# Kernel optimization log

Measured on AMD Instinct MI355X. Metric: run time of the kernel, lower is better.

## Reference

```python
import jax, jax.numpy as jnp
import numpy as np

D = 1024; NH = 16; HD = D // NH; B = 2; L = 2048
BASE_FAST = (1.0 + 5.0 ** 0.5) / 2.0
BASE_SLOW = 1618.0
BASE_GLU = 16180.0
ALPHA_ATTN = 0.42; ALPHA_MLP = 1.07; ALPHA_ADV = 1.0
H_GATE = max(8, D // 4)   # rope_gate hidden
H_NU = max(4, D // 8)     # DuplexViscosity hidden
LN_EPS = 1e-5


def _rope_cos_sin(seq_len, dim, base, dtype=jnp.float32):
    idx = jnp.arange(0, dim, 2, dtype=dtype) / float(dim)
    inv = 1.0 / (base ** idx)
    t = jnp.arange(seq_len, dtype=dtype)
    freqs = jnp.outer(t, inv)                       # (L, D/2)
    emb = jnp.concatenate([freqs, freqs], axis=-1)  # (L, D)
    return jnp.cos(emb)[None], jnp.sin(emb)[None]   # (1, L, D)


def _rotate_half(x):
    x1, x2 = jnp.split(x, 2, axis=-1)
    return jnp.concatenate([-x2, x1], axis=-1)


def _apply_rope(x, cos, sin):
    return x * cos + _rotate_half(x) * sin


def setup_inputs() -> dict:
    key = jax.random.key(0)
    ks = jax.random.split(key, 16)
    std = 0.02
    # all Linear weights stored as (in, out) so forward is x @ W + b
    return {
        "z": jax.random.normal(ks[0], (B, L, D), jnp.float32),
        "Wq": jax.random.normal(ks[1], (D, D), jnp.float32) * std,
        "bq": jnp.zeros((D,), jnp.float32),
        "Wk": jax.random.normal(ks[2], (D, D), jnp.float32) * std,
        "bk": jnp.zeros((D,), jnp.float32),
        "Wv": jax.random.normal(ks[3], (D, D), jnp.float32) * std,
        "bv": jnp.zeros((D,), jnp.float32),
        "Wcoh": jax.random.normal(ks[4], (D, D), jnp.float32) * std,
        "gamma": jnp.zeros((1,), jnp.float32),
        "rg_w1": jax.random.normal(ks[5], (D, H_GATE), jnp.float32) * std,
        "rg_b1": jnp.zeros((H_GATE,), jnp.float32),
        "rg_w2": jax.random.normal(ks[6], (H_GATE, 1), jnp.float32) * std,
        "rg_b2": jnp.zeros((1,), jnp.float32),
        "nu_diff": jnp.asarray(0.2, jnp.float32),
        "nu_adv": jnp.asarray(0.01, jnp.float32),
        "nu_w1": jax.random.normal(ks[7], (D, H_NU), jnp.float32) * std,
        "nu_b1": jnp.zeros((H_NU,), jnp.float32),
        "nu_w2": jax.random.normal(ks[8], (H_NU, 1), jnp.float32) * std,
        "nu_b2": jnp.zeros((1,), jnp.float32),
        "Wu": jax.random.normal(ks[9], (D, D), jnp.float32) * std,
        "bu": jnp.zeros((D,), jnp.float32),
        "Wg": jax.random.normal(ks[10], (D, D), jnp.float32) * std,
        "bg": jnp.zeros((D,), jnp.float32),
        "ln_w": jnp.ones((D,), jnp.float32),
        "ln_b": jnp.zeros((D,), jnp.float32),
        "Cw": jax.random.normal(ks[11], (D, D), jnp.float32) * std,
        "Cb": jnp.zeros((D,), jnp.float32),
    }


def reference(z, Wq, bq, Wk, bk, Wv, bv, Wcoh, gamma, rg_w1, rg_b1, rg_w2, rg_b2,
              nu_diff, nu_adv, nu_w1, nu_b1, nu_w2, nu_b2, Wu, bu, Wg, bg,
              ln_w, ln_b, Cw, Cb):
    b, l, d = z.shape
    dt = z.dtype
    # causal cumulative mean pool[t] = mean(z[0..t])
    pool = jnp.cumsum(z, axis=1) / jnp.arange(1, l + 1, dtype=dt)[None, :, None]

    # QKV projections
    Q = z @ Wq + bq
    K_raw = z @ Wk + bk
    V = z @ Wv + bv

    # global coherence bias: (B, Lq, Lk)
    gk = pool @ Wcoh
    gb = jnp.einsum('bld,bmd->blm', gk, K_raw) * (d ** -0.5)
    gb = jnp.tanh(gamma[0]) * gb

    # hybrid RoPE gate (small MLP on pool, exact gelu as in torch)
    gate = jax.nn.sigmoid(jax.nn.gelu(pool @ rg_w1 + rg_b1, approximate=False) @ rg_w2 + rg_b2)  # (B,L,1)
    cos_f, sin_f = _rope_cos_sin(l, d, BASE_FAST, dt)
    cos_s, sin_s = _rope_cos_sin(l, d, BASE_SLOW, dt)
    cos = gate * cos_f + (1.0 - gate) * cos_s
    sin = gate * sin_f + (1.0 - gate) * sin_s
    Qr = _apply_rope(Q, cos, sin)
    Kr = _apply_rope(K_raw, cos, sin)

    # multi-head causal attention with fused coherence bias
    Qh = Qr.reshape(b, l, NH, HD).transpose(0, 2, 1, 3)
    Kh = Kr.reshape(b, l, NH, HD).transpose(0, 2, 1, 3)
    Vh = V.reshape(b, l, NH, HD).transpose(0, 2, 1, 3)
    logits = jnp.einsum('bhld,bhmd->bhlm', Qh, Kh) * (HD ** -0.5)
    logits = logits + gb[:, None]
    causal = jnp.tril(jnp.ones((l, l), bool))
    logits = jnp.where(causal[None, None], logits, -jnp.inf)
    attn = jax.nn.softmax(logits, axis=-1)
    attn_out = jnp.einsum('bhlm,bhmd->bhld', attn, Vh).transpose(0, 2, 1, 3).reshape(b, l, d)
    attn_w = attn.mean(axis=1)

    # DuplexViscosity on causal pool
    delta = jnp.tanh(jnp.tanh(pool @ nu_w1 + nu_b1) @ nu_w2 + nu_b2) * jnp.abs(nu_adv)
    nu_b = jnp.abs(nu_diff) + delta  # (B,L,1)

    # GLU branch with fixed slow-base RoPE
    cos_g, sin_g = _rope_cos_sin(l, d, BASE_GLU, dt)
    z_glu = _apply_rope(z, cos_g, sin_g)
    bilinear = (z_glu @ Wu + bu) * (z_glu @ Wg + bg)
    adv = -(ALPHA_ADV * nu_b) * bilinear
    mu = adv.mean(axis=-1, keepdims=True)
    var = ((adv - mu) ** 2).mean(axis=-1, keepdims=True)
    adv_n = (adv - mu) * jax.lax.rsqrt(var + LN_EPS) * ln_w + ln_b
    mlp_out = adv_n @ Cw + Cb

    z_next = z + ALPHA_ATTN * attn_out + ALPHA_MLP * mlp_out
    return z_next, attn_w
```

## Files before the change

### kernel.cpp

```cpp
#include <hip/hip_runtime.h>

#define DD 1024
#define NHH 16
#define HDD 64
#define BB 2
#define LL 2048
#define MM (BB*LL)
#define HG 256
#define HN 128

#define LOG_FAST 0.48121182f
#define LOG_SLOW 7.3889461f
#define LOG_GLU  9.6915312f
#define SCL 0.18033688f

typedef __attribute__((ext_vector_type(8))) short short8;
typedef __attribute__((ext_vector_type(4))) float f32x4;

__device__ __forceinline__ float gelu_f(float x) {
    return 0.5f * x * (1.0f + erff(x * 0.70710678f));
}

__device__ __forceinline__ ushort f2b(float x) {
    unsigned u = __float_as_uint(x);
    unsigned r = (u + 0x7FFFu + ((u >> 16) & 1u)) >> 16;
    return (ushort)r;
}

__device__ __forceinline__ float b2f(ushort x) {
    return __uint_as_float(((unsigned)x) << 16);
}

__device__ __forceinline__ void gl_lds16(const ushort* g, ushort* l) {
    __builtin_amdgcn_global_load_lds(
        (const __attribute__((address_space(1))) unsigned int*)g,
        (__attribute__((address_space(3))) unsigned int*)l, 16, 0, 0);
}

#define SWZC(row, c8) (((((row) << 3) | ((c8) ^ ((row) & 7)))) << 3)

__device__ __forceinline__ void stage_tile(const ushort* gsrc, int rstride,
                                           ushort* lds, int tid) {
    int wid = tid >> 6;
#pragma unroll
    for (int r = 0; r < 2; ++r) {
        int c = r * 256 + tid;
        int row = c >> 3;
        int c8 = (c & 7) ^ (row & 7);
        gl_lds16(gsrc + (size_t)row * rstride + c8 * 8,
                 lds + (size_t)(r * 256 + wid * 64) * 8);
    }
}

#define LCH 128
#define NCH 16
__global__ void pool_scan1(const float* __restrict__ z, float* __restrict__ part,
                           float* __restrict__ ctot, ushort* __restrict__ zb) {
    int ch = blockIdx.x, dg = blockIdx.y, b = blockIdx.z;
    int d = dg * 256 + threadIdx.x;
    size_t base = ((size_t)b * LL + ch * LCH) * DD + d;
    const float* zp = z + base;
    float* pp = part + base;
    ushort* zo = zb + base;
    float s = 0.f;
    for (int t = 0; t < LCH; ++t) {
        float v = zp[(size_t)t * DD];
        s += v;
        pp[(size_t)t * DD] = s;
        zo[(size_t)t * DD] = f2b(v);
    }
    ctot[((size_t)b * NCH + ch) * DD + d] = s;
}
__global__ void pool_scan2(const float* __restrict__ part, const float* __restrict__ ctot,
                           ushort* __restrict__ poolb) {
    int ch = blockIdx.x, dg = blockIdx.y, b = blockIdx.z;
    int d = dg * 256 + threadIdx.x;
    float off = 0.f;
    for (int c = 0; c < ch; ++c) off += ctot[((size_t)b * NCH + c) * DD + d];
    int t0 = ch * LCH;
    size_t base = ((size_t)b * LL + t0) * DD + d;
    const float* pp = part + base;
    ushort* po = poolb + base;
    for (int t = 0; t < LCH; ++t) {
        po[(size_t)t * DD] = f2b((pp[(size_t)t * DD] + off) / (float)(t0 + t + 1));
    }
}

__global__ void f2bT4_kernel(const float* __restrict__ W0, const float* __restrict__ W1,
                             const float* __restrict__ W2, const float* __restrict__ W3,
                             ushort* __restrict__ Wt) {
    const float* W = blockIdx.z == 0 ? W0 : (blockIdx.z == 1 ? W1 :
                     (blockIdx.z == 2 ? W2 : W3));
    ushort* dst = Wt + (size_t)blockIdx.z * 1024 * 1024;
    __shared__ float t[32][33];
    int n0 = blockIdx.x * 32, k0 = blockIdx.y * 32;
    int tx = threadIdx.x & 31, ty = threadIdx.x >> 5;
#pragma unroll
    for (int j = 0; j < 4; ++j)
        t[ty + j * 8][tx] = W[(size_t)(k0 + ty + j * 8) * 1024 + n0 + tx];
    __syncthreads();
#pragma unroll
    for (int j = 0; j < 4; ++j)
        dst[(size_t)(n0 + ty + j * 8) * 1024 + k0 + tx] = f2b(t[tx][ty + j * 8]);
}

__global__ void f2bT_rgnu(const float* __restrict__ Wrg, const float* __restrict__ Wnu,
                          ushort* __restrict__ WtRG, ushort* __restrict__ WtNU) {
    int zc = blockIdx.z;
    if (zc == 1 && blockIdx.x >= 4) return;
    const float* W = zc == 0 ? Wrg : Wnu;
    ushort* dst = zc == 0 ? WtRG : WtNU;
    int Ndim = zc == 0 ? HG : HN;
    __shared__ float t[32][33];
    int n0 = blockIdx.x * 32, k0 = blockIdx.y * 32;
    int tx = threadIdx.x & 31, ty = threadIdx.x >> 5;
#pragma unroll
    for (int j = 0; j < 4; ++j)
        t[ty + j * 8][tx] = W[(size_t)(k0 + ty + j * 8) * Ndim + n0 + tx];
    __syncthreads();
#pragma unroll
    for (int j = 0; j < 4; ++j)
        dst[(size_t)(n0 + ty + j * 8) * 1024 + k0 + tx] = f2b(t[tx][ty + j * 8]);
}

__global__ void f2bT3_kernel(const float* __restrict__ W0, const float* __restrict__ W1,
                             const float* __restrict__ W2, ushort* __restrict__ Wt) {
    const float* W = blockIdx.z == 0 ? W0 : (blockIdx.z == 1 ? W1 : W2);
    ushort* dst = Wt + (size_t)blockIdx.z * 1024 * 1024;
    __shared__ float t[32][33];
    int n0 = blockIdx.x * 32, k0 = blockIdx.y * 32;
    int tx = threadIdx.x & 31, ty = threadIdx.x >> 5;
#pragma unroll
    for (int j = 0; j < 4; ++j)
        t[ty + j * 8][tx] = W[(size_t)(k0 + ty + j * 8) * 1024 + n0 + tx];
    __syncthreads();
#pragma unroll
    for (int j = 0; j < 4; ++j)
        dst[(size_t)(n0 + ty + j * 8) * 1024 + k0 + tx] = f2b(t[tx][ty + j * 8]);
}

__global__ __launch_bounds__(256) void gemm_mfma(
        const ushort* __restrict__ A, const ushort* __restrict__ Wt,
        const float* __restrict__ bias, float* __restrict__ C, int Ndim) {
    __shared__ ushort As[4096];
    __shared__ ushort Bs[4096];
    int tid = threadIdx.x;
    int wid = tid >> 6, lane = tid & 63;
    int n0 = blockIdx.x * 128, m0 = blockIdx.y * 128;
    int wm = wid >> 1, wn = wid & 1;
    int quad = lane >> 4, l16 = lane & 15;

    f32x4 acc[4][4];
#pragma unroll
    for (int mi = 0; mi < 4; ++mi)
#pragma unroll
        for (int ni = 0; ni < 4; ++ni) acc[mi][ni] = (f32x4){0.f, 0.f, 0.f, 0.f};

    int c0 = wid * 128 + lane;
    int c1 = c0 + 64;
    const ushort* Ag0 = A + (size_t)(m0 + (c0 & 127)) * 1024 + (c0 >> 7) * 8;
    const ushort* Ag1 = A + (size_t)(m0 + (c1 & 127)) * 1024 + (c1 >> 7) * 8;
    const ushort* Bg0 = Wt + (size_t)(n0 + (c0 & 127)) * 1024 + (c0 >> 7) * 8;
    const ushort* Bg1 = Wt + (size_t)(n0 + (c1 & 127)) * 1024 + (c1 >> 7) * 8;
    ushort* Al0 = As + wid * 1024;
    ushort* Al1 = As + wid * 1024 + 512;
    ushort* Bl0 = Bs + wid * 1024;
    ushort* Bl1 = Bs + wid * 1024 + 512;

    const ushort* a_rd = &As[(quad * 128 + wm * 64 + l16) * 8];
    const ushort* b_rd = &Bs[(quad * 128 + wn * 64 + l16) * 8];

    for (int kb = 0; kb < 1024; kb += 32) {
        gl_lds16(Ag0 + kb, Al0);
        gl_lds16(Ag1 + kb, Al1);
        gl_lds16(Bg0 + kb, Bl0);
        gl_lds16(Bg1 + kb, Bl1);
        __syncthreads();
        short8 af[4], bf[4];
#pragma unroll
        for (int mi = 0; mi < 4; ++mi)
            af[mi] = *(const short8*)(a_rd + mi * 16 * 8);
#pragma unroll
        for (int ni = 0; ni < 4; ++ni)
            bf[ni] = *(const short8*)(b_rd + ni * 16 * 8);
#pragma unroll
        for (int mi = 0; mi < 4; ++mi)
#pragma unroll
            for (int ni = 0; ni < 4; ++ni)
                acc[mi][ni] = __builtin_amdgcn_mfma_f32_16x16x32_bf16(
                    af[mi], bf[ni], acc[mi][ni], 0, 0, 0);
        __syncthreads();
    }
    int bcol[4];
    float bval[4];
#pragma unroll
    for (int ni = 0; ni < 4; ++ni) {
        bcol[ni] = n0 + wn * 64 + ni * 16 + l16;
        bval[ni] = bias ? bias[bcol[ni]] : 0.f;
    }
#pragma unroll
    for (int mi = 0; mi < 4; ++mi) {
#pragma unroll
        for (int r = 0; r < 4; ++r) {
            int row = m0 + wm * 64 + mi * 16 + quad * 4 + r;
            float* Cp = C + (size_t)row * Ndim;
#pragma unroll
            for (int ni = 0; ni < 4; ++ni)
                Cp[bcol[ni]] = acc[mi][ni][r] + bval[ni];
        }
    }
}

__global__ __launch_bounds__(256) void gemm_mfma3(
        const ushort* __restrict__ A, const ushort* __restrict__ Wt,
        const float* __restrict__ b0, const float* __restrict__ b1,
        const float* __restrict__ b2, float* __restrict__ C,
        ushort* __restrict__ K16r) {
    int zid = blockIdx.z;
    const ushort* W = Wt + (size_t)zid * 1024 * 1024;
    const float* bias = zid == 0 ? b0 : (zid == 1 ? b1 : b2);
    float* Cz = C + (size_t)zid * (size_t)MM * DD;
    __shared__ ushort As[4096];
    __shared__ ushort Bs[4096];
    int tid = threadIdx.x;
    int wid = tid >> 6, lane = tid & 63;
    int n0 = blockIdx.x * 128, m0 = blockIdx.y * 128;
    int wm = wid >> 1, wn = wid & 1;
    int quad = lane >> 4, l16 = lane & 15;

    f32x4 acc[4][4];
#pragma unroll
    for (int mi = 0; mi < 4; ++mi)
#pragma unroll
        for (int ni = 0; ni < 4; ++ni) acc[mi][ni] = (f32x4){0.f, 0.f, 0.f, 0.f};

    int c0 = wid * 128 + lane;
    int c1 = c0 + 64;
    const ushort* Ag0 = A + (size_t)(m0 + (c0 & 127)) * 1024 + (c0 >> 7) * 8;
    const ushort* Ag1 = A + (size_t)(m0 + (c1 & 127)) * 1024 + (c1 >> 7) * 8;
    const ushort* Bg0 = W + (size_t)(n0 + (c0 & 127)) * 1024 + (c0 >> 7) * 8;
    const ushort* Bg1 = W + (size_t)(n0 + (c1 & 127)) * 1024 + (c1 >> 7) * 8;
    ushort* Al0 = As + wid * 1024;
    ushort* Al1 = As + wid * 1024 + 512;
    ushort* Bl0 = Bs + wid * 1024;
    ushort* Bl1 = Bs + wid * 1024 + 512;

    const ushort* a_rd = &As[(quad * 128 + wm * 64 + l16) * 8];
    const ushort* b_rd = &Bs[(quad * 128 + wn * 64 + l16) * 8];

    for (int kb = 0; kb < 1024; kb += 32) {
        gl_lds16(Ag0 + kb, Al0);
        gl_lds16(Ag1 + kb, Al1);
        gl_lds16(Bg0 + kb, Bl0);
        gl_lds16(Bg1 + kb, Bl1);
        __syncthreads();
        short8 af[4], bf[4];
#pragma unroll
        for (int mi = 0; mi < 4; ++mi)
            af[mi] = *(const short8*)(a_rd + mi * 16 * 8);
#pragma unroll
        for (int ni = 0; ni < 4; ++ni)
            bf[ni] = *(const short8*)(b_rd + ni * 16 * 8);
#pragma unroll
        for (int mi = 0; mi < 4; ++mi)
#pragma unroll
            for (int ni = 0; ni < 4; ++ni)
                acc[mi][ni] = __builtin_amdgcn_mfma_f32_16x16x32_bf16(
                    af[mi], bf[ni], acc[mi][ni], 0, 0, 0);
        __syncthreads();
    }
    float bval[4];
    int bcol[4];
#pragma unroll
    for (int ni = 0; ni < 4; ++ni) {
        bcol[ni] = n0 + wn * 64 + ni * 16 + l16;
        bval[ni] = bias[bcol[ni]];
    }
    bool doK = (zid == 1) && (K16r != nullptr);
#pragma unroll
    for (int mi = 0; mi < 4; ++mi) {
#pragma unroll
        for (int r = 0; r < 4; ++r) {
            int row = m0 + wm * 64 + mi * 16 + quad * 4 + r;
            float* Cp = Cz + (size_t)row * 1024;
            ushort* Kp = K16r + (size_t)row * 1024;
#pragma unroll
            for (int ni = 0; ni < 4; ++ni) {
                float v = acc[mi][ni][r] + bval[ni];
                Cp[bcol[ni]] = v;
                if (doK) Kp[bcol[ni]] = f2b(v);
            }
        }
    }
}

__global__ __launch_bounds__(256) void gemm_mfma_b16out(
        const ushort* __restrict__ A, const ushort* __restrict__ Wt,
        ushort* __restrict__ C, int Ndim) {
    __shared__ ushort As[4096];
    __shared__ ushort Bs[4096];
    int tid = threadIdx.x;
    int wid = tid >> 6, lane = tid & 63;
    int n0 = blockIdx.x * 128, m0 = blockIdx.y * 128;
    int wm = wid >> 1, wn = wid & 1;
    int quad = lane >> 4, l16 = lane & 15;

    f32x4 acc[4][4];
#pragma unroll
    for (int mi = 0; mi < 4; ++mi)
#pragma unroll
        for (int ni = 0; ni < 4; ++ni) acc[mi][ni] = (f32x4){0.f, 0.f, 0.f, 0.f};

    int c0 = wid * 128 + lane;
    int c1 = c0 + 64;
    const ushort* Ag0 = A + (size_t)(m0 + (c0 & 127)) * 1024 + (c0 >> 7) * 8;
    const ushort* Ag1 = A + (size_t)(m0 + (c1 & 127)) * 1024 + (c1 >> 7) * 8;
    const ushort* Bg0 = Wt + (size_t)(n0 + (c0 & 127)) * 1024 + (c0 >> 7) * 8;
    const ushort* Bg1 = Wt + (size_t)(n0 + (c1 & 127)) * 1024 + (c1 >> 7) * 8;
    ushort* Al0 = As + wid * 1024;
    ushort* Al1 = As + wid * 1024 + 512;
    ushort* Bl0 = Bs + wid * 1024;
    ushort* Bl1 = Bs + wid * 1024 + 512;

    const ushort* a_rd = &As[(quad * 128 + wm * 64 + l16) * 8];
    const ushort* b_rd = &Bs[(quad * 128 + wn * 64 + l16) * 8];

    for (int kb = 0; kb < 1024; kb += 32) {
        gl_lds16(Ag0 + kb, Al0);
        gl_lds16(Ag1 + kb, Al1);
        gl_lds16(Bg0 + kb, Bl0);
        gl_lds16(Bg1 + kb, Bl1);
        __syncthreads();
        short8 af[4], bf[4];
#pragma unroll
        for (int mi = 0; mi < 4; ++mi)
            af[mi] = *(const short8*)(a_rd + mi * 16 * 8);
#pragma unroll
        for (int ni = 0; ni < 4; ++ni)
            bf[ni] = *(const short8*)(b_rd + ni * 16 * 8);
#pragma unroll
        for (int mi = 0; mi < 4; ++mi)
#pragma unroll
            for (int ni = 0; ni < 4; ++ni)
                acc[mi][ni] = __builtin_amdgcn_mfma_f32_16x16x32_bf16(
                    af[mi], bf[ni], acc[mi][ni], 0, 0, 0);
        __syncthreads();
    }
#pragma unroll
    for (int mi = 0; mi < 4; ++mi) {
#pragma unroll
        for (int r = 0; r < 4; ++r) {
            int row = m0 + wm * 64 + mi * 16 + quad * 4 + r;
            ushort* Cp = C + (size_t)row * Ndim;
#pragma unroll
            for (int ni = 0; ni < 4; ++ni)
                Cp[n0 + wn * 64 + ni * 16 + l16] = f2b(acc[mi][ni][r]);
        }
    }
}

__global__ __launch_bounds__(256) void gemm_gates(
        const ushort* __restrict__ A, const ushort* __restrict__ WtRG,
        const ushort* __restrict__ WtNU, const float* __restrict__ rg_b1,
        const float* __restrict__ nu_b1, float* __restrict__ H1,
        float* __restrict__ N1) {
    int bx = blockIdx.x;
    bool isH = bx < 2;
    const ushort* Wt = isH ? WtRG : WtNU;
    const float* bias = isH ? rg_b1 : nu_b1;
    float* C = isH ? H1 : N1;
    int Ndim = isH ? HG : HN;
    int n0 = isH ? bx * 128 : 0;
    int m0 = blockIdx.y * 128;
    __shared__ ushort As[4096];
    __shared__ ushort Bs[4096];
    int tid = threadIdx.x;
    int wid = tid >> 6, lane = tid & 63;
    int wm = wid >> 1, wn = wid & 1;
    int quad = lane >> 4, l16 = lane & 15;

    f32x4 acc[4][4];
#pragma unroll
    for (int mi = 0; mi < 4; ++mi)
#pragma unroll
        for (int ni = 0; ni < 4; ++ni) acc[mi][ni] = (f32x4){0.f, 0.f, 0.f, 0.f};

    int c0 = wid * 128 + lane;
    int c1 = c0 + 64;
    const ushort* Ag0 = A + (size_t)(m0 + (c0 & 127)) * 1024 + (c0 >> 7) * 8;
    const ushort* Ag1 = A + (size_t)(m0 + (c1 & 127)) * 1024 + (c1 >> 7) * 8;
    const ushort* Bg0 = Wt + (size_t)(n0 + (c0 & 127)) * 1024 + (c0 >> 7) * 8;
    const ushort* Bg1 = Wt + (size_t)(n0 + (c1 & 127)) * 1024 + (c1 >> 7) * 8;
    ushort* Al0 = As + wid * 1024;
    ushort* Al1 = As + wid * 1024 + 512;
    ushort* Bl0 = Bs + wid * 1024;
    ushort* Bl1 = Bs + wid * 1024 + 512;

    const ushort* a_rd = &As[(quad * 128 + wm * 64 + l16) * 8];
    const ushort* b_rd = &Bs[(quad * 128 + wn * 64 + l16) * 8];

    for (int kb = 0; kb < 1024; kb += 32) {
        gl_lds16(Ag0 + kb, Al0);
        gl_lds16(Ag1 + kb, Al1);
        gl_lds16(Bg0 + kb, Bl0);
        gl_lds16(Bg1 + kb, Bl1);
        __syncthreads();
        short8 af[4], bf[4];
#pragma unroll
        for (int mi = 0; mi < 4; ++mi)
            af[mi] = *(const short8*)(a_rd + mi * 16 * 8);
#pragma unroll
        for (int ni = 0; ni < 4; ++ni)
            bf[ni] = *(const short8*)(b_rd + ni * 16 * 8);
#pragma unroll
        for (int mi = 0; mi < 4; ++mi)
#pragma unroll
            for (int ni = 0; ni < 4; ++ni)
                acc[mi][ni] = __builtin_amdgcn_mfma_f32_16x16x32_bf16(
                    af[mi], bf[ni], acc[mi][ni], 0, 0, 0);
        __syncthreads();
    }
    int bcol[4];
    float bval[4];
#pragma unroll
    for (int ni = 0; ni < 4; ++ni) {
        bcol[ni] = n0 + wn * 64 + ni * 16 + l16;
        bval[ni] = bias[bcol[ni]];
    }
#pragma unroll
    for (int mi = 0; mi < 4; ++mi) {
#pragma unroll
        for (int r = 0; r < 4; ++r) {
            int row = m0 + wm * 64 + mi * 16 + quad * 4 + r;
            float* Cp = C + (size_t)row * Ndim;
#pragma unroll
            for (int ni = 0; ni < 4; ++ni)
                Cp[bcol[ni]] = acc[mi][ni][r] + bval[ni];
        }
    }
}

__global__ __launch_bounds__(256) void gb_mfma(
        const ushort* __restrict__ gk16, const ushort* __restrict__ K16r,
        const float* __restrict__ gamma, ushort* __restrict__ gb) {
    int lt = blockIdx.x >> 4, mt = blockIdx.x & 15;
    if (mt > lt) return;
    int b = blockIdx.y;
    __shared__ ushort As[4096];
    __shared__ ushort Bs[4096];
    int tid = threadIdx.x;
    int wid = tid >> 6, lane = tid & 63;
    int l0 = lt * 128, m0 = mt * 128;
    int wm = wid >> 1, wn = wid & 1;
    int quad = lane >> 4, l16 = lane & 15;

    f32x4 acc[4][4];
#pragma unroll
    for (int mi = 0; mi < 4; ++mi)
#pragma unroll
        for (int ni = 0; ni < 4; ++ni) acc[mi][ni] = (f32x4){0.f, 0.f, 0.f, 0.f};

    int c0 = wid * 128 + lane;
    int c1 = c0 + 64;
    const ushort* Ag0 = gk16 + ((size_t)b * LL + l0 + (c0 & 127)) * 1024 + (c0 >> 7) * 8;
    const ushort* Ag1 = gk16 + ((size_t)b * LL + l0 + (c1 & 127)) * 1024 + (c1 >> 7) * 8;
    const ushort* Bg0 = K16r + ((size_t)b * LL + m0 + (c0 & 127)) * 1024 + (c0 >> 7) * 8;
    const ushort* Bg1 = K16r + ((size_t)b * LL + m0 + (c1 & 127)) * 1024 + (c1 >> 7) * 8;
    ushort* Al0 = As + wid * 1024;
    ushort* Al1 = As + wid * 1024 + 512;
    ushort* Bl0 = Bs + wid * 1024;
    ushort* Bl1 = Bs + wid * 1024 + 512;

    const ushort* a_rd = &As[(quad * 128 + wm * 64 + l16) * 8];
    const ushort* b_rd = &Bs[(quad * 128 + wn * 64 + l16) * 8];

    for (int kb = 0; kb < 1024; kb += 32) {
        gl_lds16(Ag0 + kb, Al0);
        gl_lds16(Ag1 + kb, Al1);
        gl_lds16(Bg0 + kb, Bl0);
        gl_lds16(Bg1 + kb, Bl1);
        __syncthreads();
        short8 af[4], bf[4];
#pragma unroll
        for (int mi = 0; mi < 4; ++mi)
            af[mi] = *(const short8*)(a_rd + mi * 16 * 8);
#pragma unroll
        for (int ni = 0; ni < 4; ++ni)
            bf[ni] = *(const short8*)(b_rd + ni * 16 * 8);
#pragma unroll
        for (int mi = 0; mi < 4; ++mi)
#pragma unroll
            for (int ni = 0; ni < 4; ++ni)
                acc[mi][ni] = __builtin_amdgcn_mfma_f32_16x16x32_bf16(
                    af[mi], bf[ni], acc[mi][ni], 0, 0, 0);
        __syncthreads();
    }
    float scale = tanhf(gamma[0]) * 0.25f;
#pragma unroll
    for (int mi = 0; mi < 4; ++mi) {
#pragma unroll
        for (int r = 0; r < 4; ++r) {
            int row = l0 + wm * 64 + mi * 16 + quad * 4 + r;
            ushort* Cp = gb + ((size_t)b * LL + row) * LL;
#pragma unroll
            for (int ni = 0; ni < 4; ++ni)
                Cp[m0 + wn * 64 + ni * 16 + l16] = f2b(acc[mi][ni][r] * scale);
        }
    }
}

__global__ __launch_bounds__(256) void gatenu_fin(
        const float* __restrict__ H1, const float* __restrict__ N1,
        const float* __restrict__ rg_w2, const float* __restrict__ rg_b2,
        const float* __restrict__ nu_w2, const float* __restrict__ nu_b2,
        const float* __restrict__ nu_diff, const float* __restrict__ nu_adv,
        float* __restrict__ gate, float* __restrict__ nub) {
    int row = blockIdx.x, tid = threadIdx.x;
    float gv = gelu_f(H1[(size_t)row * HG + tid]) * rg_w2[tid];
    float nv = (tid < HN) ? tanhf(N1[(size_t)row * HN + tid]) * nu_w2[tid] : 0.f;
    for (int off = 32; off; off >>= 1) {
        gv += __shfl_down(gv, off);
        nv += __shfl_down(nv, off);
    }
    __shared__ float pg[4], pn[4];
    if ((tid & 63) == 0) { pg[tid >> 6] = gv; pn[tid >> 6] = nv; }
    __syncthreads();
    if (tid == 0) {
        float ga = pg[0] + pg[1] + pg[2] + pg[3] + rg_b2[0];
        gate[row] = 1.f / (1.f + expf(-ga));
        float na = pn[0] + pn[1] + pn[2] + pn[3] + nu_b2[0];
        nub[row] = fabsf(nu_diff[0]) + tanhf(na) * fabsf(nu_adv[0]);
    }
}

__global__ void rope_qk_bf16(const float* __restrict__ Q, const float* __restrict__ K,
                             const float* __restrict__ gate,
                             ushort* __restrict__ Q16, ushort* __restrict__ K16) {
    int idx = blockIdx.x * 256 + threadIdx.x;
    int row = idx >> 9;
    int i = idx & 511;
    int b = row >> 11, t = row & (LL - 1);
    float g = gate[row];
    float fi = (float)i * (1.0f / 512.0f);
    float tf = (float)t;
    float af = tf * expf(-fi * LOG_FAST);
    float as = tf * expf(-fi * LOG_SLOW);
    float c = g * cosf(af) + (1.f - g) * cosf(as);
    float s = g * sinf(af) + (1.f - g) * sinf(as);
    size_t base = (size_t)row * DD;
    float x = Q[base + i], y = Q[base + 512 + i];
    float q1 = x * c - y * s, q2 = y * c + x * s;
    x = K[base + i]; y = K[base + 512 + i];
    float k1 = x * c - y * s, k2 = y * c + x * s;
    int h1 = i >> 6, d1 = i & 63;
    size_t o1 = ((size_t)(b * 16 + h1) * LL + t) * 64 + d1;
    size_t o2 = ((size_t)(b * 16 + 8 + h1) * LL + t) * 64 + d1;
    Q16[o1] = f2b(q1); Q16[o2] = f2b(q2);
    K16[o1] = f2b(k1); K16[o2] = f2b(k2);
}

__global__ __launch_bounds__(256) void vt16_kernel(const float* __restrict__ V,
                                                   ushort* __restrict__ VT) {
    __shared__ ushort t[64][72];
    int lb = blockIdx.x, hb = blockIdx.y, b = blockIdx.z;
    int tid = threadIdx.x;
    {
        int l = tid >> 2, c0 = (tid & 3) * 16;
        const float* Vp = V + ((size_t)(b * LL) + lb * 64 + l) * DD + hb * 64 + c0;
#pragma unroll
        for (int j = 0; j < 4; ++j) {
            float4 v = *(const float4*)(Vp + j * 4);
            t[l][c0 + j * 4 + 0] = f2b(v.x);
            t[l][c0 + j * 4 + 1] = f2b(v.y);
            t[l][c0 + j * 4 + 2] = f2b(v.z);
            t[l][c0 + j * 4 + 3] = f2b(v.w);
        }
    }
    __syncthreads();
    {
        int d = tid >> 2, l0 = (tid & 3) * 16;
        ushort tmp[16];
#pragma unroll
        for (int j = 0; j < 16; ++j) tmp[j] = t[l0 + j][d];
        ushort* Op = VT + ((size_t)((b * 16 + hb) * 64) + d) * LL + lb * 64 + l0;
        *(ushort4*)(Op + 0)  = *(ushort4*)&tmp[0];
        *(ushort4*)(Op + 4)  = *(ushort4*)&tmp[4];
        *(ushort4*)(Op + 8)  = *(ushort4*)&tmp[8];
        *(ushort4*)(Op + 12) = *(ushort4*)&tmp[12];
    }
}

__global__ void rope_glu_b16(const float* __restrict__ z, ushort* __restrict__ zg) {
    int idx = blockIdx.x * 256 + threadIdx.x;
    int row = idx >> 9;
    int i = idx & 511;
    int t = row & (LL - 1);
    float fi = (float)i * (1.0f / 512.0f);
    float ag = (float)t * expf(-fi * LOG_GLU);
    float c = cosf(ag), s = sinf(ag);
    size_t base = (size_t)row * DD;
    float x = z[base + i], y = z[base + 512 + i];
    zg[base + i]       = f2b(x * c - y * s);
    zg[base + 512 + i] = f2b(y * c + x * s);
}

__global__ __launch_bounds__(256, 4) void attn_flash_mfma(
        const ushort* __restrict__ Q16, const ushort* __restrict__ K16,
        const ushort* __restrict__ VT16, const ushort* __restrict__ gb16,
        float* __restrict__ attn_out, float* __restrict__ stats) {
    int h = blockIdx.x, qt = 31 - blockIdx.y, b = blockIdx.z;
    __shared__ ushort QP[4608];
    __shared__ ushort Ks[2][4096];
    __shared__ ushort Vs[4096];
    int tid = threadIdx.x, wid = tid >> 6, lane = tid & 63;
    int quad = lane >> 4, l16 = lane & 15;
    const ushort* Qg = Q16 + ((size_t)(b * 16 + h) * LL) * 64;
    const ushort* Kg = K16 + ((size_t)(b * 16 + h) * LL) * 64;
    const ushort* Vg = VT16 + ((size_t)(b * 16 + h) * 64) * LL;
    const ushort* gbB = gb16 + (size_t)b * LL * LL;
    float* stB = stats + ((size_t)(b * 16 + h) * LL) * 2;
    int qrow = wid * 16 + quad * 4;
    int q0 = qt * 64;

    stage_tile(Qg + (size_t)q0 * 64, 64, QP, tid);
    stage_tile(Kg, 64, Ks[0], tid);
    stage_tile(Vg, LL, Vs, tid);
    __syncthreads();
    short8 qf[2];
#pragma unroll
    for (int ks = 0; ks < 2; ++ks)
        qf[ks] = *(const short8*)(QP + SWZC(wid * 16 + l16, ks * 4 + quad));
    __syncthreads();
    ushort* Pw = QP + wid * 1152;

    short ov = (l16 == 0) ? (short)0x3F80 : (short)0;
    short8 onesf = {ov, ov, ov, ov, ov, ov, ov, ov};

    f32x4 ofr[5];
    float m_r[4];
#pragma unroll
    for (int nt = 0; nt < 5; ++nt) ofr[nt] = (f32x4){0.f, 0.f, 0.f, 0.f};
#pragma unroll
    for (int r = 0; r < 4; ++r) m_r[r] = -3e38f;

    for (int kt = 0; kt <= qt; ++kt) {
        int cur = kt & 1;
        int k0 = kt * 64;
        ushort gw[4][4];
#pragma unroll
        for (int r = 0; r < 4; ++r) {
            const ushort* gp = gbB + (size_t)(q0 + qrow + r) * LL + k0 + l16;
#pragma unroll
            for (int nt = 0; nt < 4; ++nt) gw[nt][r] = gp[nt * 16];
        }
        if (kt > 0) stage_tile(Vg + k0, LL, Vs, tid);
        if (kt < qt) stage_tile(Kg + (size_t)(k0 + 64) * 64, 64, Ks[cur ^ 1], tid);

        f32x4 sf[4];
#pragma unroll
        for (int nt = 0; nt < 4; ++nt)
#pragma unroll
            for (int r = 0; r < 4; ++r) sf[nt][r] = b2f(gw[nt][r]);
#pragma unroll
        for (int ks = 0; ks < 2; ++ks)
#pragma unroll
            for (int nt = 0; nt < 4; ++nt) {
                short8 kf = *(const short8*)(Ks[cur] + SWZC(nt * 16 + l16, ks * 4 + quad));
                sf[nt] = __builtin_amdgcn_mfma_f32_16x16x32_bf16(qf[ks], kf, sf[nt], 0, 0, 0);
            }
        if (kt == qt) {
#pragma unroll
            for (int nt = 0; nt < 4; ++nt)
#pragma unroll
                for (int r = 0; r < 4; ++r)
                    if (nt * 16 + l16 > qrow + r) sf[nt][r] = -1e30f;
        }
        float alpha[4], mS[4];
#pragma unroll
        for (int r = 0; r < 4; ++r) {
            float m = fmaxf(fmaxf(sf[0][r], sf[1][r]), fmaxf(sf[2][r], sf[3][r]));
#pragma unroll
            for (int off = 1; off < 16; off <<= 1)
                m = fmaxf(m, __shfl_xor(m, off));
            float nm = fmaxf(m_r[r], m);
            alpha[r] = __builtin_amdgcn_exp2f((m_r[r] - nm) * SCL);
            m_r[r] = nm;
            mS[r] = nm * SCL;
        }
#pragma unroll
        for (int nt = 0; nt < 4; ++nt)
#pragma unroll
            for (int r = 0; r < 4; ++r) {
                float p = __builtin_amdgcn_exp2f(fmaf(sf[nt][r], SCL, -mS[r]));
                Pw[(quad * 4 + r) * 72 + nt * 16 + l16] = f2b(p);
            }
#pragma unroll
        for (int nt = 0; nt < 5; ++nt)
#pragma unroll
            for (int r = 0; r < 4; ++r) ofr[nt][r] *= alpha[r];
        short8 pf[2];
#pragma unroll
        for (int ks = 0; ks < 2; ++ks)
            pf[ks] = *(const short8*)(Pw + l16 * 72 + ks * 32 + quad * 8);
#pragma unroll
        for (int ks = 0; ks < 2; ++ks) {
#pragma unroll
            for (int nt = 0; nt < 4; ++nt) {
                short8 vf = *(const short8*)(Vs + SWZC(nt * 16 + l16, ks * 4 + quad));
                ofr[nt] = __builtin_amdgcn_mfma_f32_16x16x32_bf16(pf[ks], vf, ofr[nt], 0, 0, 0);
            }
            ofr[4] = __builtin_amdgcn_mfma_f32_16x16x32_bf16(pf[ks], onesf, ofr[4], 0, 0, 0);
        }
        __syncthreads();
    }
#pragma unroll
    for (int r = 0; r < 4; ++r) {
        float l = __shfl(ofr[4][r], (lane & 48));
        float rinv = 1.0f / l;
        float* op = attn_out + ((size_t)(b * LL) + q0 + qrow + r) * DD + h * 64 + l16;
#pragma unroll
        for (int nt = 0; nt < 4; ++nt)
            op[nt * 16] = ofr[nt][r] * rinv;
    }
    if (l16 == 0) {
#pragma unroll
        for (int r = 0; r < 4; ++r) {
            size_t si = (size_t)(q0 + qrow + r) * 2;
            stB[si]     = m_r[r];
            stB[si + 1] = ofr[4][r];
        }
    }
}

__global__ __launch_bounds__(256, 4) void attn_w_mfma(
        const ushort* __restrict__ Q16, const ushort* __restrict__ K16,
        const ushort* __restrict__ gb16, const float* __restrict__ stats,
        float* __restrict__ aw) {
    int qt = blockIdx.x >> 5, kt = blockIdx.x & 31;
    int b = blockIdx.y;
    int tid = threadIdx.x, wid = tid >> 6, lane = tid & 63;
    int quad = lane >> 4, l16 = lane & 15;
    int q0 = qt * 64, k0 = kt * 64;
    int qrow = wid * 16 + quad * 4;
    if (kt > qt) {
        int rr = tid >> 2, c0 = (tid & 3) * 16;
        float4 zv = make_float4(0.f, 0.f, 0.f, 0.f);
        float* p = aw + ((size_t)(b * LL) + q0 + rr) * LL + k0 + c0;
#pragma unroll
        for (int j = 0; j < 4; ++j) *(float4*)(p + j * 4) = zv;
        return;
    }
    __shared__ ushort Qs[2][4096], Ks[2][4096];
    float acc[4][4];
#pragma unroll
    for (int nt = 0; nt < 4; ++nt)
#pragma unroll
        for (int r = 0; r < 4; ++r) acc[nt][r] = 0.f;
    f32x4 gacc[4];
    const ushort* gbB = gb16 + (size_t)b * LL * LL;
#pragma unroll
    for (int r = 0; r < 4; ++r) {
        const ushort* gp = gbB + (size_t)(q0 + qrow + r) * LL + k0 + l16;
#pragma unroll
        for (int nt = 0; nt < 4; ++nt) gacc[nt][r] = b2f(gp[nt * 16]);
    }
    bool diag = (kt == qt);
    stage_tile(Q16 + ((size_t)(b * 16) * LL + q0) * 64, 64, Qs[0], tid);
    stage_tile(K16 + ((size_t)(b * 16) * LL + k0) * 64, 64, Ks[0], tid);
    __syncthreads();
    for (int h = 0; h < NHH; ++h) {
        int cur = h & 1;
        float mS[4], li[4];
        const float* sp = stats + ((size_t)(b * 16 + h) * LL + q0 + qrow) * 2;
#pragma unroll
        for (int r = 0; r < 4; ++r) {
            mS[r] = sp[r * 2] * SCL;
            li[r] = 1.0f / sp[r * 2 + 1];
        }
        if (h < 15) {
            stage_tile(Q16 + ((size_t)(b * 16 + h + 1) * LL + q0) * 64, 64, Qs[cur ^ 1], tid);
            stage_tile(K16 + ((size_t)(b * 16 + h + 1) * LL + k0) * 64, 64, Ks[cur ^ 1], tid);
        }
        short8 qf[2];
#pragma unroll
        for (int ks = 0; ks < 2; ++ks)
            qf[ks] = *(const short8*)(Qs[cur] + SWZC(wid * 16 + l16, ks * 4 + quad));
        f32x4 sf[4];
#pragma unroll
        for (int nt = 0; nt < 4; ++nt) sf[nt] = gacc[nt];
#pragma unroll
        for (int ks = 0; ks < 2; ++ks)
#pragma unroll
            for (int nt = 0; nt < 4; ++nt) {
                short8 kf = *(const short8*)(Ks[cur] + SWZC(nt * 16 + l16, ks * 4 + quad));
                sf[nt] = __builtin_amdgcn_mfma_f32_16x16x32_bf16(qf[ks], kf, sf[nt], 0, 0, 0);
            }
#pragma unroll
        for (int nt = 0; nt < 4; ++nt)
#pragma unroll
            for (int r = 0; r < 4; ++r) {
                int row = qrow + r;
                if (!diag || (nt * 16 + l16 <= row))
                    acc[nt][r] += __builtin_amdgcn_exp2f(fmaf(sf[nt][r], SCL, -mS[r])) * li[r];
            }
        __syncthreads();
    }
#pragma unroll
    for (int r = 0; r < 4; ++r) {
        float* op = aw + ((size_t)(b * LL) + q0 + qrow + r) * LL + k0 + l16;
#pragma unroll
        for (int nt = 0; nt < 4; ++nt)
            op[nt * 16] = acc[nt][r] * 0.0625f;
    }
}

__global__ __launch_bounds__(256) void adv_ln_kernel(
        const float* __restrict__ U, const float* __restrict__ G,
        const float* __restrict__ nub, const float* __restrict__ lnw,
        const float* __restrict__ lnb, ushort* __restrict__ out) {
    int row = blockIdx.x, tid = threadIdx.x;
    size_t base = (size_t)row * DD + tid * 4;
    float4 u4 = *(const float4*)&U[base];
    float4 g4 = *(const float4*)&G[base];
    float nu = nub[row];
    float a[4];
    a[0] = -nu * u4.x * g4.x;
    a[1] = -nu * u4.y * g4.y;
    a[2] = -nu * u4.z * g4.z;
    a[3] = -nu * u4.w * g4.w;
    float ts = a[0] + a[1] + a[2] + a[3];
    float tq = a[0] * a[0] + a[1] * a[1] + a[2] * a[2] + a[3] * a[3];
    for (int off = 32; off; off >>= 1) {
        ts += __shfl_down(ts, off);
        tq += __shfl_down(tq, off);
    }
    __shared__ float r1[4], r2[4];
    if ((tid & 63) == 0) { r1[tid >> 6] = ts; r2[tid >> 6] = tq; }
    __syncthreads();
    __shared__ float s_mu, s_rs;
    if (tid == 0) {
        float S  = r1[0] + r1[1] + r1[2] + r1[3];
        float Qq = r2[0] + r2[1] + r2[2] + r2[3];
        float mu = S * (1.0f / 1024.f);
        float var = Qq * (1.0f / 1024.f) - mu * mu;
        s_mu = mu;
        s_rs = rsqrtf(var + 1e-5f);
    }
    __syncthreads();
    float mu = s_mu, rs = s_rs;
    float4 w4 = *(const float4*)&lnw[tid * 4];
    float4 b4 = *(const float4*)&lnb[tid * 4];
    ushort4 ov;
    ov.x = f2b((a[0] - mu) * rs * w4.x + b4.x);
    ov.y = f2b((a[1] - mu) * rs * w4.y + b4.y);
    ov.z = f2b((a[2] - mu) * rs * w4.z + b4.z);
    ov.w = f2b((a[3] - mu) * rs * w4.w + b4.w);
    *(ushort4*)&out[base] = ov;
}

__global__ void final_kernel(const float* __restrict__ z, const float* __restrict__ ao,
                             const float* __restrict__ mlp, float* __restrict__ out) {
    size_t i = ((size_t)blockIdx.x * 256 + threadIdx.x) * 4;
    float4 z4 = *(const float4*)&z[i];
    float4 a4 = *(const float4*)&ao[i];
    float4 m4 = *(const float4*)&mlp[i];
    float4 o;
    o.x = z4.x + 0.42f * a4.x + 1.07f * m4.x;
    o.y = z4.y + 0.42f * a4.y + 1.07f * m4.y;
    o.z = z4.z + 0.42f * a4.z + 1.07f * m4.z;
    o.w = z4.w + 0.42f * a4.w + 1.07f * m4.w;
    *(float4*)&out[i] = o;
}

extern "C" void kernel_launch(void* const* d_in, const int* in_sizes, int n_in,
                              void* d_out, int out_size, void* d_ws, size_t ws_size,
                              hipStream_t stream) {
    const float* z       = (const float*)d_in[0];
    const float* Wq      = (const float*)d_in[1];
    const float* bq      = (const float*)d_in[2];
    const float* Wk      = (const float*)d_in[3];
    const float* bk      = (const float*)d_in[4];
    const float* Wv      = (const float*)d_in[5];
    const float* bv      = (const float*)d_in[6];
    const float* Wcoh    = (const float*)d_in[7];
    const float* gamma   = (const float*)d_in[8];
    const float* rg_w1   = (const float*)d_in[9];
    const float* rg_b1   = (const float*)d_in[10];
    const float* rg_w2   = (const float*)d_in[11];
    const float* rg_b2   = (const float*)d_in[12];
    const float* nu_diff = (const float*)d_in[13];
    const float* nu_adv  = (const float*)d_in[14];
    const float* nu_w1   = (const float*)d_in[15];
    const float* nu_b1   = (const float*)d_in[16];
    const float* nu_w2   = (const float*)d_in[17];
    const float* nu_b2   = (const float*)d_in[18];
    const float* Wu      = (const float*)d_in[19];
    const float* bu      = (const float*)d_in[20];
    const float* Wg      = (const float*)d_in[21];
    const float* bg      = (const float*)d_in[22];
    const float* ln_w    = (const float*)d_in[23];
    const float* ln_b    = (const float*)d_in[24];
    const float* Cw      = (const float*)d_in[25];
    const float* Cb      = (const float*)d_in[26];

    float* out_z  = (float*)d_out;
    float* out_aw = out_z + (size_t)MM * DD;

    float* ws = (float*)d_ws;
    const size_t MD = (size_t)MM * DD;
    float* pool  = ws;
    float* Qb    = ws + MD;
    float* Kb    = ws + 2 * MD;
    float* Vb    = ws + 3 * MD;
    float* gkb   = ws + 4 * MD;
    float* gbb   = ws + 5 * MD;
    float* H1    = ws + 7 * MD;
    float* N1    = H1 + (size_t)MM * HG;
    float* gate  = N1 + (size_t)MM * HN;
    float* nub   = gate + MM;
    float* stats = nub + MM;
    float* ctot  = stats + (size_t)BB * NHH * LL * 2;

    char* gbase  = (char*)gbb;
    ushort* Ab   = (ushort*)gbase;
    ushort* Wb   = (ushort*)(gbase + (size_t)8 * 1024 * 1024);
    ushort* gb16 = (ushort*)(gbase + (size_t)16 * 1024 * 1024);
    ushort* WtRG = Wb;
    ushort* WtNU = Wb + (size_t)1024 * 1024;
    ushort* Q16  = (ushort*)Vb;
    ushort* K16  = (ushort*)Vb + MD;
    ushort* VT16 = (ushort*)pool;
    ushort* poolb = (ushort*)pool;
    float*  part = gkb;
    ushort* gk16 = (ushort*)gkb;
    ushort* K16r = (ushort*)gkb + MD;

    dim3 g128(8, 32);
    dim3 wT_g(32, 32);

    pool_scan1<<<dim3(NCH, 4, BB), 256, 0, stream>>>(z, part, ctot, Ab);
    pool_scan2<<<dim3(NCH, 4, BB), 256, 0, stream>>>(part, ctot, poolb);
    f2bT4_kernel<<<dim3(32, 32, 4), 256, 0, stream>>>(Wq, Wk, Wv, Wcoh, Wb);
    gemm_mfma3<<<dim3(8, 32, 3), 256, 0, stream>>>(Ab, Wb, bq, bk, bv, Qb, K16r);
    gemm_mfma_b16out<<<g128, 256, 0, stream>>>(poolb, Wb + (size_t)3 * 1024 * 1024, gk16, DD);
    f2bT_rgnu<<<dim3(8, 32, 2), 256, 0, stream>>>(rg_w1, nu_w1, WtRG, WtNU);
    gemm_gates<<<dim3(3, 32), 256, 0, stream>>>(poolb, WtRG, WtNU, rg_b1, nu_b1, H1, N1);
    gb_mfma<<<dim3(256, BB), 256, 0, stream>>>(gk16, K16r, gamma, gb16);
    gatenu_fin<<<dim3(MM), 256, 0, stream>>>(H1, N1, rg_w2, rg_b2, nu_w2, nu_b2,
                                             nu_diff, nu_adv, gate, nub);
    vt16_kernel<<<dim3(32, 16, BB), 256, 0, stream>>>(Vb, VT16);
    rope_qk_bf16<<<dim3((MM * 512) / 256), 256, 0, stream>>>(Qb, Kb, gate, Q16, K16);
    attn_flash_mfma<<<dim3(NHH, 32, BB), 256, 0, stream>>>(Q16, K16, VT16, gb16, gkb, stats);
    attn_w_mfma<<<dim3(1024, BB), 256, 0, stream>>>(Q16, K16, gb16, stats, out_aw);
    rope_glu_b16<<<dim3((MM * 512) / 256), 256, 0, stream>>>(z, Ab);
    f2bT3_kernel<<<dim3(32, 32, 3), 256, 0, stream>>>(Wu, Wg, Cw, Wb);
    gemm_mfma3<<<dim3(8, 32, 2), 256, 0, stream>>>(Ab, Wb, bu, bg, bg, Qb, nullptr);
    adv_ln_kernel<<<dim3(MM), 256, 0, stream>>>(Qb, Kb, nub, ln_w, ln_b, Ab);
    gemm_mfma<<<g128, 256, 0, stream>>>(Ab, Wb + (size_t)2 * 1024 * 1024, Cb, Qb, DD);
    final_kernel<<<dim3(MD / 4 / 256), 256, 0, stream>>>(z, gkb, Qb, out_z);
}
```

Before: 581.5 us.

## Double-buffer K/V in flash attention and vectorize gate-bias tile accesses

The flash-attention kernel now double-buffers both the K and V tiles in shared memory. It loads Q fragments straight from global memory into registers, loads V fragments into registers before issuing the next tile's stage, and swizzles the P scratch buffer. The gate-bias matrix is now written and read as ushort4 using a permuted column order inside each 64-column tile, so the gate-bias kernel, the flash kernel and the attention-weights kernel all had to change consistently. MFMA sections are wrapped in setprio hints, and the loops are unrolled two phases at a time. Shared memory per block grows and register pressure rises in exchange for fewer scattered 2-byte accesses and better overlap of global loads with compute.

```diff
diff --git a/kernel.cpp b/kernel.cpp
--- a/kernel.cpp
+++ b/kernel.cpp
@@ -502,9 +502,12 @@
         for (int r = 0; r < 4; ++r) {
             int row = l0 + wm * 64 + mi * 16 + quad * 4 + r;
             ushort* Cp = gb + ((size_t)b * LL + row) * LL;
-#pragma unroll
-            for (int ni = 0; ni < 4; ++ni)
-                Cp[m0 + wn * 64 + ni * 16 + l16] = f2b(acc[mi][ni][r] * scale);
+            ushort4 o;
+            o.x = f2b(acc[mi][0][r] * scale);
+            o.y = f2b(acc[mi][1][r] * scale);
+            o.z = f2b(acc[mi][2][r] * scale);
+            o.w = f2b(acc[mi][3][r] * scale);
+            *(ushort4*)(Cp + m0 + wn * 64 + l16 * 4) = o;
         }
     }
 }
@@ -609,9 +612,11 @@
         const ushort* __restrict__ VT16, const ushort* __restrict__ gb16,
         float* __restrict__ attn_out, float* __restrict__ stats) {
     int h = blockIdx.x, qt = 31 - blockIdx.y, b = blockIdx.z;
-    __shared__ ushort QP[4608];
-    __shared__ ushort Ks[2][4096];
-    __shared__ ushort Vs[4096];
+    __shared__ ushort Ks0[4096];
+    __shared__ ushort Vs0[4096];
+    __shared__ ushort Ks1[4096];
+    __shared__ ushort Vs1[4096];
+    __shared__ ushort Ps[4096];
     int tid = threadIdx.x, wid = tid >> 6, lane = tid & 63;
     int quad = lane >> 4, l16 = lane & 15;
     const ushort* Qg = Q16 + ((size_t)(b * 16 + h) * LL) * 64;
@@ -622,16 +627,17 @@
     int qrow = wid * 16 + quad * 4;
     int q0 = qt * 64;
 
-    stage_tile(Qg + (size_t)q0 * 64, 64, QP, tid);
-    stage_tile(Kg, 64, Ks[0], tid);
-    stage_tile(Vg, LL, Vs, tid);
+    short8 qf[2];
+    {
+        const ushort* qp = Qg + (size_t)(q0 + wid * 16 + l16) * 64 + quad * 8;
+        qf[0] = *(const short8*)(qp);
+        qf[1] = *(const short8*)(qp + 32);
+    }
+    stage_tile(Kg, 64, Ks0, tid);
+    stage_tile(Vg, LL, Vs0, tid);
     __syncthreads();
-    short8 qf[2];
-#pragma unroll
-    for (int ks = 0; ks < 2; ++ks)
-        qf[ks] = *(const short8*)(QP + SWZC(wid * 16 + l16, ks * 4 + quad));
-    __syncthreads();
-    ushort* Pw = QP + wid * 1152;
+
+    ushort* Pw = Ps + wid * 1024;
 
     short ov = (l16 == 0) ? (short)0x3F80 : (short)0;
     short8 onesf = {ov, ov, ov, ov, ov, ov, ov, ov};
@@ -643,76 +649,91 @@
 #pragma unroll
     for (int r = 0; r < 4; ++r) m_r[r] = -3e38f;
 
-    for (int kt = 0; kt <= qt; ++kt) {
-        int cur = kt & 1;
-        int k0 = kt * 64;
-        ushort gw[4][4];
-#pragma unroll
-        for (int r = 0; r < 4; ++r) {
-            const ushort* gp = gbB + (size_t)(q0 + qrow + r) * LL + k0 + l16;
-#pragma unroll
-            for (int nt = 0; nt < 4; ++nt) gw[nt][r] = gp[nt * 16];
-        }
-        if (kt > 0) stage_tile(Vg + k0, LL, Vs, tid);
-        if (kt < qt) stage_tile(Kg + (size_t)(k0 + 64) * 64, 64, Ks[cur ^ 1], tid);
-
-        f32x4 sf[4];
-#pragma unroll
-        for (int nt = 0; nt < 4; ++nt)
-#pragma unroll
-            for (int r = 0; r < 4; ++r) sf[nt][r] = b2f(gw[nt][r]);
-#pragma unroll
-        for (int ks = 0; ks < 2; ++ks)
-#pragma unroll
-            for (int nt = 0; nt < 4; ++nt) {
-                short8 kf = *(const short8*)(Ks[cur] + SWZC(nt * 16 + l16, ks * 4 + quad));
-                sf[nt] = __builtin_amdgcn_mfma_f32_16x16x32_bf16(qf[ks], kf, sf[nt], 0, 0, 0);
-            }
-        if (kt == qt) {
-#pragma unroll
-            for (int nt = 0; nt < 4; ++nt)
-#pragma unroll
-                for (int r = 0; r < 4; ++r)
-                    if (nt * 16 + l16 > qrow + r) sf[nt][r] = -1e30f;
-        }
-        float alpha[4], mS[4];
-#pragma unroll
-        for (int r = 0; r < 4; ++r) {
-            float m = fmaxf(fmaxf(sf[0][r], sf[1][r]), fmaxf(sf[2][r], sf[3][r]));
-#pragma unroll
-            for (int off = 1; off < 16; off <<= 1)
-                m = fmaxf(m, __shfl_xor(m, off));
-            float nm = fmaxf(m_r[r], m);
-            alpha[r] = __builtin_amdgcn_exp2f((m_r[r] - nm) * SCL);
-            m_r[r] = nm;
-            mS[r] = nm * SCL;
-        }
-#pragma unroll
-        for (int nt = 0; nt < 4; ++nt)
-#pragma unroll
-            for (int r = 0; r < 4; ++r) {
-                float p = __builtin_amdgcn_exp2f(fmaf(sf[nt][r], SCL, -mS[r]));
-                Pw[(quad * 4 + r) * 72 + nt * 16 + l16] = f2b(p);
-            }
-#pragma unroll
-        for (int nt = 0; nt < 5; ++nt)
-#pragma unroll
-            for (int r = 0; r < 4; ++r) ofr[nt][r] *= alpha[r];
-        short8 pf[2];
-#pragma unroll
-        for (int ks = 0; ks < 2; ++ks)
-            pf[ks] = *(const short8*)(Pw + l16 * 72 + ks * 32 + quad * 8);
-#pragma unroll
-        for (int ks = 0; ks < 2; ++ks) {
-#pragma unroll
-            for (int nt = 0; nt < 4; ++nt) {
-                short8 vf = *(const short8*)(Vs + SWZC(nt * 16 + l16, ks * 4 + quad));
-                ofr[nt] = __builtin_amdgcn_mfma_f32_16x16x32_bf16(pf[ks], vf, ofr[nt], 0, 0, 0);
-            }
-            ofr[4] = __builtin_amdgcn_mfma_f32_16x16x32_bf16(pf[ks], onesf, ofr[4], 0, 0, 0);
-        }
-        __syncthreads();
-    }
+#define FLASH_PHASE(KC, VC, KN, VN, T) do {                                       \
+    int k0_ = (T) * 64;                                                           \
+    ushort4 gw_[4];                                                               \
+    _Pragma("unroll")                                                             \
+    for (int r = 0; r < 4; ++r)                                                   \
+        gw_[r] = *(const ushort4*)(gbB + (size_t)(q0 + qrow + r) * LL + k0_ + l16 * 4); \
+    f32x4 sf_[4];                                                                 \
+    _Pragma("unroll")                                                             \
+    for (int nt = 0; nt < 4; ++nt) sf_[nt] = (f32x4){0.f, 0.f, 0.f, 0.f};         \
+    _Pragma("unroll")                                                             \
+    for (int ks = 0; ks < 2; ++ks)                                                \
+        _Pragma("unroll")                                                         \
+        for (int nt = 0; nt < 4; ++nt) {                                          \
+            short8 kf_ = *(const short8*)((KC) + SWZC(nt * 16 + l16, ks * 4 + quad)); \
+            sf_[nt] = __builtin_amdgcn_mfma_f32_16x16x32_bf16(qf[ks], kf_, sf_[nt], 0, 0, 0); \
+        }                                                                         \
+    short8 vf_[2][4];                                                             \
+    _Pragma("unroll")                                                             \
+    for (int ks = 0; ks < 2; ++ks)                                                \
+        _Pragma("unroll")                                                         \
+        for (int nt = 0; nt < 4; ++nt)                                            \
+            vf_[ks][nt] = *(const short8*)((VC) + SWZC(nt * 16 + l16, ks * 4 + quad)); \
+    if ((T) + 1 <= qt) {                                                          \
+        stage_tile(Kg + (size_t)(k0_ + 64) * 64, 64, (KN), tid);                  \
+        stage_tile(Vg + (k0_ + 64), LL, (VN), tid);                               \
+    }                                                                             \
+    _Pragma("unroll")                                                             \
+    for (int r = 0; r < 4; ++r) {                                                 \
+        sf_[0][r] += b2f(gw_[r].x); sf_[1][r] += b2f(gw_[r].y);                   \
+        sf_[2][r] += b2f(gw_[r].z); sf_[3][r] += b2f(gw_[r].w);                   \
+    }                                                                             \
+    if ((T) == qt) {                                                              \
+        _Pragma("unroll")                                                         \
+        for (int nt = 0; nt < 4; ++nt)                                            \
+            _Pragma("unroll")                                                     \
+            for (int r = 0; r < 4; ++r)                                           \
+                if (nt * 16 + l16 > qrow + r) sf_[nt][r] = -1e30f;                \
+    }                                                                             \
+    float alpha_[4], mS_[4];                                                      \
+    _Pragma("unroll")                                                             \
+    for (int r = 0; r < 4; ++r) {                                                 \
+        float m_ = fmaxf(fmaxf(sf_[0][r], sf_[1][r]), fmaxf(sf_[2][r], sf_[3][r])); \
+        _Pragma("unroll")                                                         \
+        for (int off = 1; off < 16; off <<= 1)                                    \
+            m_ = fmaxf(m_, __shfl_xor(m_, off));                                  \
+        float nm_ = fmaxf(m_r[r], m_);                                            \
+        alpha_[r] = __builtin_amdgcn_exp2f((m_r[r] - nm_) * SCL);                 \
+        m_r[r] = nm_;                                                             \
+        mS_[r] = nm_ * SCL;                                                       \
+    }                                                                             \
+    _Pragma("unroll")                                                             \
+    for (int nt = 0; nt < 4; ++nt)                                                \
+        _Pragma("unroll")                                                         \
+        for (int r = 0; r < 4; ++r) {                                             \
+            float p_ = __builtin_amdgcn_exp2f(fmaf(sf_[nt][r], SCL, -mS_[r]));    \
+            int prow_ = quad * 4 + r;                                             \
+            int chk_ = (nt * 2) | (l16 >> 3);                                     \
+            Pw[prow_ * 64 + ((chk_ ^ (prow_ & 7)) << 3) + (l16 & 7)] = f2b(p_);   \
+        }                                                                         \
+    _Pragma("unroll")                                                             \
+    for (int nt = 0; nt < 5; ++nt)                                                \
+        _Pragma("unroll")                                                         \
+        for (int r = 0; r < 4; ++r) ofr[nt][r] *= alpha_[r];                      \
+    short8 pf_[2];                                                                \
+    _Pragma("unroll")                                                             \
+    for (int ks = 0; ks < 2; ++ks)                                                \
+        pf_[ks] = *(const short8*)(Pw + l16 * 64 + (((ks * 4 + quad) ^ (l16 & 7)) << 3)); \
+    __builtin_amdgcn_s_setprio(1);                                                \
+    _Pragma("unroll")                                                             \
+    for (int ks = 0; ks < 2; ++ks) {                                              \
+        _Pragma("unroll")                                                         \
+        for (int nt = 0; nt < 4; ++nt)                                            \
+            ofr[nt] = __builtin_amdgcn_mfma_f32_16x16x32_bf16(pf_[ks], vf_[ks][nt], ofr[nt], 0, 0, 0); \
+        ofr[4] = __builtin_amdgcn_mfma_f32_16x16x32_bf16(pf_[ks], onesf, ofr[4], 0, 0, 0); \
+    }                                                                             \
+    __builtin_amdgcn_s_setprio(0);                                                \
+    __syncthreads();                                                              \
+} while (0)
+
+    for (int kt = 0; kt <= qt; kt += 2) {
+        FLASH_PHASE(Ks0, Vs0, Ks1, Vs1, kt);
+        if (kt + 1 <= qt) FLASH_PHASE(Ks1, Vs1, Ks0, Vs0, kt + 1);
+    }
+#undef FLASH_PHASE
+
 #pragma unroll
     for (int r = 0; r < 4; ++r) {
         float l = __shfl(ofr[4][r], (lane & 48));
@@ -750,7 +771,10 @@
         for (int j = 0; j < 4; ++j) *(float4*)(p + j * 4) = zv;
         return;
     }
-    __shared__ ushort Qs[2][4096], Ks[2][4096];
+    __shared__ ushort Qs0[4096];
+    __shared__ ushort Ks0[4096];
+    __shared__ ushort Qs1[4096];
+    __shared__ ushort Ks1[4096];
     float acc[4][4];
 #pragma unroll
     for (int nt = 0; nt < 4; ++nt)
@@ -760,51 +784,67 @@
     const ushort* gbB = gb16 + (size_t)b * LL * LL;
 #pragma unroll
     for (int r = 0; r < 4; ++r) {
-        const ushort* gp = gbB + (size_t)(q0 + qrow + r) * LL + k0 + l16;
-#pragma unroll
-        for (int nt = 0; nt < 4; ++nt) gacc[nt][r] = b2f(gp[nt * 16]);
+        ushort4 g4 = *(const ushort4*)(gbB + (size_t)(q0 + qrow + r) * LL + k0 + l16 * 4);
+        gacc[0][r] = b2f(g4.x);
+        gacc[1][r] = b2f(g4.y);
+        gacc[2][r] = b2f(g4.z);
+        gacc[3][r] = b2f(g4.w);
     }
     bool diag = (kt == qt);
-    stage_tile(Q16 + ((size_t)(b * 16) * LL + q0) * 64, 64, Qs[0], tid);
-    stage_tile(K16 + ((size_t)(b * 16) * LL + k0) * 64, 64, Ks[0], tid);
+    stage_tile(Q16 + ((size_t)(b * 16) * LL + q0) * 64, 64, Qs0, tid);
+    stage_tile(K16 + ((size_t)(b * 16) * LL + k0) * 64, 64, Ks0, tid);
     __syncthreads();
-    for (int h = 0; h < NHH; ++h) {
-        int cur = h & 1;
-        float mS[4], li[4];
-        const float* sp = stats + ((size_t)(b * 16 + h) * LL + q0 + qrow) * 2;
-#pragma unroll
-        for (int r = 0; r < 4; ++r) {
-            mS[r] = sp[r * 2] * SCL;
-            li[r] = 1.0f / sp[r * 2 + 1];
-        }
-        if (h < 15) {
-            stage_tile(Q16 + ((size_t)(b * 16 + h + 1) * LL + q0) * 64, 64, Qs[cur ^ 1], tid);
-            stage_tile(K16 + ((size_t)(b * 16 + h + 1) * LL + k0) * 64, 64, Ks[cur ^ 1], tid);
-        }
-        short8 qf[2];
-#pragma unroll
-        for (int ks = 0; ks < 2; ++ks)
-            qf[ks] = *(const short8*)(Qs[cur] + SWZC(wid * 16 + l16, ks * 4 + quad));
-        f32x4 sf[4];
-#pragma unroll
-        for (int nt = 0; nt < 4; ++nt) sf[nt] = gacc[nt];
-#pragma unroll
-        for (int ks = 0; ks < 2; ++ks)
-#pragma unroll
-            for (int nt = 0; nt < 4; ++nt) {
-                short8 kf = *(const short8*)(Ks[cur] + SWZC(nt * 16 + l16, ks * 4 + quad));
-                sf[nt] = __builtin_amdgcn_mfma_f32_16x16x32_bf16(qf[ks], kf, sf[nt], 0, 0, 0);
-            }
-#pragma unroll
-        for (int nt = 0; nt < 4; ++nt)
-#pragma unroll
-            for (int r = 0; r < 4; ++r) {
-                int row = qrow + r;
-                if (!diag || (nt * 16 + l16 <= row))
-                    acc[nt][r] += __builtin_amdgcn_exp2f(fmaf(sf[nt][r], SCL, -mS[r])) * li[r];
-            }
-        __syncthreads();
-    }
+
+#define AW_PHASE(QC, KC, QN, KN, H) do {                                          \
+    short8 qf_[2], kf_[2][4];                                                     \
+    _Pragma("unroll")                                                             \
+    for (int ks = 0; ks < 2; ++ks)                                                \
+        qf_[ks] = *(const short8*)((QC) + SWZC(wid * 16 + l16, ks * 4 + quad));   \
+    _Pragma("unroll")                                                             \
+    for (int ks = 0; ks < 2; ++ks)                                                \
+        _Pragma("unroll")                                                         \
+        for (int nt = 0; nt < 4; ++nt)                                            \
+            kf_[ks][nt] = *(const short8*)((KC) + SWZC(nt * 16 + l16, ks * 4 + quad)); \
+    if ((H) < 15) {                                                               \
+        stage_tile(Q16 + ((size_t)(b * 16 + (H) + 1) * LL + q0) * 64, 64, (QN), tid); \
+        stage_tile(K16 + ((size_t)(b * 16 + (H) + 1) * LL + k0) * 64, 64, (KN), tid); \
+    }                                                                             \
+    float mS_[4], li_[4];                                                         \
+    {                                                                             \
+        const float* sp_ = stats + ((size_t)(b * 16 + (H)) * LL + q0 + qrow) * 2; \
+        _Pragma("unroll")                                                         \
+        for (int r = 0; r < 4; ++r) {                                             \
+            mS_[r] = sp_[r * 2] * SCL;                                            \
+            li_[r] = 1.0f / sp_[r * 2 + 1];                                       \
+        }                                                                         \
+    }                                                                             \
+    f32x4 sf_[4];                                                                 \
+    _Pragma("unroll")                                                             \
+    for (int nt = 0; nt < 4; ++nt) sf_[nt] = gacc[nt];                            \
+    __builtin_amdgcn_s_setprio(1);                                                \
+    _Pragma("unroll")                                                             \
+    for (int ks = 0; ks < 2; ++ks)                                                \
+        _Pragma("unroll")                                                         \
+        for (int nt = 0; nt < 4; ++nt)                                            \
+            sf_[nt] = __builtin_amdgcn_mfma_f32_16x16x32_bf16(qf_[ks], kf_[ks][nt], sf_[nt], 0, 0, 0); \
+    __builtin_amdgcn_s_setprio(0);                                                \
+    _Pragma("unroll")                                                             \
+    for (int nt = 0; nt < 4; ++nt)                                                \
+        _Pragma("unroll")                                                         \
+        for (int r = 0; r < 4; ++r) {                                             \
+            int row_ = qrow + r;                                                  \
+            if (!diag || (nt * 16 + l16 <= row_))                                 \
+                acc[nt][r] += __builtin_amdgcn_exp2f(fmaf(sf_[nt][r], SCL, -mS_[r])) * li_[r]; \
+        }                                                                         \
+    __syncthreads();                                                              \
+} while (0)
+
+    for (int h = 0; h < NHH; h += 2) {
+        AW_PHASE(Qs0, Ks0, Qs1, Ks1, h);
+        AW_PHASE(Qs1, Ks1, Qs0, Ks0, h + 1);
+    }
+#undef AW_PHASE
+
 #pragma unroll
     for (int r = 0; r < 4; ++r) {
         float* op = aw + ((size_t)(b * LL) + q0 + qrow + r) * LL + k0 + l16;
```

Measured after the change: 654.2 us. +12.5%, slower.
